# Kernel tuning notes

Measured on AMD Instinct MI355X. Metric: run time of the kernel, lower is better.

The kernel has to match this reference:

```python
import jax, jax.numpy as jnp
import numpy as np

V, D, H, L, S, B, HD, FF, MAXS = 50257, 1024, 8, 6, 1024, 2, 128, 4096, 2048
EPS = 1e-5
STD = 0.02


def rmsnorm(x, w):
    rms = jnp.sqrt(jnp.mean(x * x, axis=-1, keepdims=True) + EPS)
    return w * (x / rms)


def setup_inputs() -> dict:
    key = jax.random.key(0)
    ks = jax.random.split(key, 9)
    return {
        "tokens": jax.random.randint(ks[0], (S, B), 0, V),
        "tok_emb": STD * jax.random.normal(ks[1], (V, D), jnp.float32),
        "pos_emb": STD * jax.random.normal(ks[2], (MAXS, D), jnp.float32),
        "attn_norm_w": jnp.ones((L, D), jnp.float32),
        "Wq": STD * jax.random.normal(ks[3], (L, H, D, HD), jnp.float32),
        "Wk": STD * jax.random.normal(ks[4], (L, H, D, HD), jnp.float32),
        "Wv": STD * jax.random.normal(ks[5], (L, H, D, HD), jnp.float32),
        "Wo": STD * jax.random.normal(ks[6], (L, H, HD, D), jnp.float32),
        "mlp_norm_w": jnp.ones((L, D), jnp.float32),
        "W1": STD * jax.random.normal(ks[7], (L, D, FF), jnp.float32),
        "W2": STD * jax.random.normal(ks[8], (L, FF, D), jnp.float32),
        "final_norm_w": jnp.ones((D,), jnp.float32),
    }


def reference(tokens, tok_emb, pos_emb, attn_norm_w, Wq, Wk, Wv, Wo,
              mlp_norm_w, W1, W2, final_norm_w):
    seq_len = tokens.shape[0]
    scale = HD ** -0.5
    # (S, B, D) token + learned positional embeddings
    x = tok_emb[tokens] + pos_emb[:seq_len][:, None, :]
    causal = jnp.tril(jnp.ones((seq_len, seq_len), bool))  # (S, S)
    for l in range(L):
        n = rmsnorm(x, attn_norm_w[l])
        q = jnp.einsum('sbd,hdk->bhsk', n, Wq[l])
        k = jnp.einsum('sbd,hdk->bhsk', n, Wk[l])
        v = jnp.einsum('sbd,hdk->bhsk', n, Wv[l])
        scores = jnp.einsum('bhsk,bhtk->bhst', q, k) * scale
        scores = jnp.where(causal, scores, -jnp.inf)
        w = jax.nn.softmax(scores, axis=-1)
        attn = jnp.einsum('bhst,bhtk->bhsk', w, v)
        # per-head out_proj summed over heads (matches sum over head modules)
        x = x + jnp.einsum('bhsk,hkd->sbd', attn, Wo[l])
        m = rmsnorm(x, mlp_norm_w[l])
        h = jax.nn.silu(jnp.einsum('sbd,df->sbf', m, W1[l]))
        x = x + jnp.einsum('sbf,fd->sbd', h, W2[l])
    x = rmsnorm(x, final_norm_w)
    logits = jnp.einsum('sbd,vd->sbv', x, tok_emb)  # tied lm_head
    return logits
```

## Files before the change

kernel.cpp:

```cpp
#include <hip/hip_runtime.h>
#include <hip/hip_bf16.h>
#include <cstddef>
#include <cstdint>

#define VOCAB 50257
#define VPAD  50432
#define DMODEL 1024
#define NHEAD 8
#define NLAYER 6
#define SEQ 1024
#define BATCH 2
#define HDIM 128
#define FFDIM 4096
#define NTOK (SEQ * BATCH)
#define QKVLD 3072
#define EPSV 1e-5f


typedef __attribute__((ext_vector_type(8))) short short8;
typedef __attribute__((ext_vector_type(4))) float f32x4;

__device__ __forceinline__ unsigned short f2bf(float f) {
    union { float f; unsigned u; } v; v.f = f;
    unsigned r = v.u + 0x7FFF + ((v.u >> 16) & 1);
    return (unsigned short)(r >> 16);
}

__global__ __launch_bounds__(256) void embed_kernel(
    const int* __restrict__ tokens, const float* __restrict__ tok_emb,
    const float* __restrict__ pos_emb, float* __restrict__ x)
{
    int idx = blockIdx.x * 256 + threadIdx.x;
    int t = idx >> 10;
    int d = idx & (DMODEL - 1);
    int b = t >> 10, s = t & (SEQ - 1);
    int tok = tokens[s * BATCH + b];
    x[idx] = tok_emb[(size_t)tok * DMODEL + d] + pos_emb[(size_t)s * DMODEL + d];
}

__global__ __launch_bounds__(256) void rmsnorm_bf_kernel(
    const float* __restrict__ x, const float* __restrict__ w,
    unsigned short* __restrict__ o)
{
    int t = blockIdx.x;
    int tid = threadIdx.x;
    const float4 xv = ((const float4*)(x + (size_t)t * DMODEL))[tid];
    float ss = xv.x * xv.x + xv.y * xv.y + xv.z * xv.z + xv.w * xv.w;
    __shared__ float red[256];
    red[tid] = ss;
    __syncthreads();
    for (int off = 128; off > 0; off >>= 1) {
        if (tid < off) red[tid] += red[tid + off];
        __syncthreads();
    }
    float inv = rsqrtf(red[0] * (1.0f / DMODEL) + EPSV);
    const float4 wv = ((const float4*)w)[tid];
    ushort4 ov;
    ov.x = f2bf(wv.x * xv.x * inv);
    ov.y = f2bf(wv.y * xv.y * inv);
    ov.z = f2bf(wv.z * xv.z * inv);
    ov.w = f2bf(wv.w * xv.w * inv);
    ((ushort4*)(o + (size_t)t * DMODEL))[tid] = ov;
}

__global__ __launch_bounds__(256) void transpose_cast_kernel(
    const float* __restrict__ in, unsigned short* __restrict__ out, int R, int C)
{
    __shared__ float tile[32][33];
    const size_t bo = (size_t)blockIdx.z * R * C;
    const float* src = in + bo;
    unsigned short* dst = out + bo;
    int c0 = blockIdx.x * 32, r0 = blockIdx.y * 32;
    int tx = threadIdx.x, ty = threadIdx.y;
    #pragma unroll
    for (int i = 0; i < 32; i += 8)
        tile[ty + i][tx] = src[(size_t)(r0 + ty + i) * C + c0 + tx];
    __syncthreads();
    #pragma unroll
    for (int i = 0; i < 32; i += 8)
        dst[(size_t)(c0 + ty + i) * R + r0 + tx] = f2bf(tile[tx][ty + i]);
}

__global__ __launch_bounds__(256) void transpose_qkv_kernel(
    const float* __restrict__ in, unsigned short* __restrict__ out, int row_off)
{
    __shared__ float tile[32][33];
    int z = blockIdx.z;
    int l = z >> 3, h = z & 7;
    const float* src = in + (size_t)z * DMODEL * HDIM;
    unsigned short* dst = out + (size_t)l * QKVLD * DMODEL
                              + (size_t)(row_off + h * HDIM) * DMODEL;
    int c0 = blockIdx.x * 32, r0 = blockIdx.y * 32;
    int tx = threadIdx.x, ty = threadIdx.y;
    #pragma unroll
    for (int i = 0; i < 32; i += 8)
        tile[ty + i][tx] = src[(size_t)(r0 + ty + i) * HDIM + c0 + tx];
    __syncthreads();
    #pragma unroll
    for (int i = 0; i < 32; i += 8)
        dst[(size_t)(c0 + ty + i) * DMODEL + r0 + tx] = f2bf(tile[tx][ty + i]);
}

__global__ __launch_bounds__(256) void vt_transpose_kernel(
    const unsigned short* __restrict__ qkv, unsigned short* __restrict__ vt)
{
    __shared__ unsigned short tile[32][33];
    int c0 = blockIdx.x * 32;
    int r0 = blockIdx.y * 32;
    int tx = threadIdx.x, ty = threadIdx.y;
    #pragma unroll
    for (int i = 0; i < 32; i += 8)
        tile[ty + i][tx] = qkv[(size_t)(r0 + ty + i) * QKVLD + 2048 + c0 + tx];
    __syncthreads();
    #pragma unroll
    for (int i = 0; i < 32; i += 8)
        vt[(size_t)(c0 + ty + i) * NTOK + r0 + tx] = tile[tx][ty + i];
}

__global__ __launch_bounds__(256) void cast_pad_kernel(
    const float* __restrict__ in, unsigned short* __restrict__ out,
    long n_src, long n_tot)
{
    long i = ((long)blockIdx.x * 256 + threadIdx.x) * 8;
    if (i >= n_tot) return;
    short8 o8;
    if (i < n_src) {
        const float4* p = (const float4*)(in + i);
        float4 a = p[0], b = p[1];
        o8[0] = (short)f2bf(a.x); o8[1] = (short)f2bf(a.y);
        o8[2] = (short)f2bf(a.z); o8[3] = (short)f2bf(a.w);
        o8[4] = (short)f2bf(b.x); o8[5] = (short)f2bf(b.y);
        o8[6] = (short)f2bf(b.z); o8[7] = (short)f2bf(b.w);
    } else {
        o8 = (short8)0;
    }
    *(short8*)(out + i) = o8;
}

template<bool ATOMIC, bool SILU, bool BF16OUT>
__global__ __launch_bounds__(256, 2) void mm128_kernel(
    const unsigned short* __restrict__ A, const unsigned short* __restrict__ Bt,
    void* __restrict__ Cv, int M, int N, int K, int rows, int ksplit)
{
    int nwg = gridDim.x;
    int flat = blockIdx.x;
    int q8 = nwg >> 3, r8 = nwg & 7;
    int xcd = flat & 7, lid = flat >> 3;
    int wg = (r8 == 0) ? (xcd * q8 + lid)
           : ((xcd < r8 ? xcd * (q8 + 1) : r8 * (q8 + 1) + (xcd - r8) * q8) + lid);
    int rs = rows * ksplit;
    const int col0 = (wg / rs) * 128;
    int rem = wg % rs;
    const int row0 = (rem / ksplit) * 128;
    const int sk   = rem % ksplit;
    const int Keff = K / ksplit;
    const int kbase = sk * Keff;

    __shared__ __align__(16) char lds[65536];
    const int tid  = threadIdx.x;
    const int lane = tid & 63;
    const int wave = tid >> 6;
    const int wm = wave >> 1, wn = wave & 1;
    const int g  = lane >> 4;
    const int c  = lane & 15;

    f32x4 acc[4][4] = {};

    auto STAGE = [&](int buf, int t) {
        const int k0 = kbase + t * 64;
        char* base = lds + buf * 32768;
        #pragma unroll
        for (int j = 0; j < 4; ++j) {
            int chunk = j * 256 + tid;
            int row = chunk >> 3, slot = chunk & 7;
            int ss = slot ^ (row & 7);
            __builtin_amdgcn_global_load_lds(
                (const __attribute__((address_space(1))) void*)
                    (A + (size_t)(row0 + row) * K + k0 + ss * 8),
                (__attribute__((address_space(3))) void*)(base + chunk * 16), 16, 0, 0);
        }
        #pragma unroll
        for (int j = 0; j < 4; ++j) {
            int chunk = j * 256 + tid;
            int row = chunk >> 3, slot = chunk & 7;
            int ss = slot ^ (row & 7);
            __builtin_amdgcn_global_load_lds(
                (const __attribute__((address_space(1))) void*)
                    (Bt + (size_t)(col0 + row) * K + k0 + ss * 8),
                (__attribute__((address_space(3))) void*)(base + 16384 + chunk * 16), 16, 0, 0);
        }
    };

    const int NT = Keff >> 6;
    STAGE(0, 0);
    asm volatile("s_waitcnt vmcnt(0)" ::: "memory");
    __builtin_amdgcn_s_barrier();
    __builtin_amdgcn_sched_barrier(0);

    for (int t = 0; t < NT; ++t) {
        if (t + 1 < NT) STAGE((t + 1) & 1, t + 1);

        char* base = lds + (t & 1) * 32768;
        short8 af[2][4], bf[2][4];
        #pragma unroll
        for (int ks = 0; ks < 2; ++ks) {
            #pragma unroll
            for (int i = 0; i < 4; ++i) {
                int rowa = wm * 64 + i * 16 + c;
                af[ks][i] = *(const short8*)(base + rowa * 128 + (((ks * 4 + g) ^ (rowa & 7)) << 4));
                int rowb = wn * 64 + i * 16 + c;
                bf[ks][i] = *(const short8*)(base + 16384 + rowb * 128 + (((ks * 4 + g) ^ (rowb & 7)) << 4));
            }
        }
        __builtin_amdgcn_s_setprio(1);
        #pragma unroll
        for (int ks = 0; ks < 2; ++ks)
            #pragma unroll
            for (int i = 0; i < 4; ++i)
                #pragma unroll
                for (int j = 0; j < 4; ++j)
                    acc[i][j] = __builtin_amdgcn_mfma_f32_16x16x32_bf16(
                        af[ks][i], bf[ks][j], acc[i][j], 0, 0, 0);
        __builtin_amdgcn_s_setprio(0);

        if (t + 1 < NT) asm volatile("s_waitcnt vmcnt(0)" ::: "memory");
        __builtin_amdgcn_s_barrier();
        __builtin_amdgcn_sched_barrier(0);
    }

    float* Cf = (float*)Cv;
    unsigned short* Cb = (unsigned short*)Cv;
    const int crow  = row0 + wm * 64 + g * 4;
    const int ccol0 = col0 + wn * 64 + c;
    #pragma unroll
    for (int i = 0; i < 4; ++i) {
        #pragma unroll
        for (int j = 0; j < 4; ++j) {
            int gcol = ccol0 + j * 16;
            #pragma unroll
            for (int r = 0; r < 4; ++r) {
                int grow = crow + i * 16 + r;
                float v = acc[i][j][r];
                if (SILU) v = v / (1.0f + __expf(-v));
                size_t ci = (size_t)grow * N + gcol;
                if (ATOMIC)       atomicAdd(&Cf[ci], v);
                else if (BF16OUT) Cb[ci] = f2bf(v);
                else              Cf[ci] = v;
            }
        }
    }
}

template<bool SILU, bool BF16OUT, int RM>
__global__ __launch_bounds__(512, 1) void mm256_kernel(
    const unsigned short* __restrict__ A, const unsigned short* __restrict__ Bt,
    void* __restrict__ Cv, int M, int N, int K, int rows)
{
    int nwg = gridDim.x;
    int flat = blockIdx.x;
    int q8 = nwg >> 3, r8 = nwg & 7;
    int xcd = flat & 7, lid = flat >> 3;
    int wg = (r8 == 0) ? (xcd * q8 + lid)
           : ((xcd < r8 ? xcd * (q8 + 1) : r8 * (q8 + 1) + (xcd - r8) * q8) + lid);
    const int row0 = (wg % rows) * 256;
    const int col0 = (wg / rows) * 256;

    __shared__ __align__(16) char lds[131072];
    const int tid  = threadIdx.x;
    const int lane = tid & 63;
    const int wave = tid >> 6;
    const int wm = wave >> 2;
    const int wn = wave & 3;
    const int g  = lane >> 4;
    const int c  = lane & 15;

    f32x4 acc[8][4] = {};

    auto STAGE = [&](int buf, int tile) {
        const int k0 = tile * 32;
        char* base = lds + buf * 32768;
        #pragma unroll
        for (int j = 0; j < 2; ++j) {
            int chunk = j * 512 + tid;
            int row = chunk >> 2, slot = chunk & 3;
            int sslot = slot ^ ((row >> 1) & 3);
            __builtin_amdgcn_global_load_lds(
                (const __attribute__((address_space(1))) void*)
                    (A + (size_t)(row0 + row) * K + k0 + sslot * 8),
                (__attribute__((address_space(3))) void*)(base + chunk * 16), 16, 0, 0);
        }
        #pragma unroll
        for (int j = 0; j < 2; ++j) {
            int chunk = j * 512 + tid;
            int row = chunk >> 2, slot = chunk & 3;
            int sslot = slot ^ ((row >> 1) & 3);
            __builtin_amdgcn_global_load_lds(
                (const __attribute__((address_space(1))) void*)
                    (Bt + (size_t)(col0 + row) * K + k0 + sslot * 8),
                (__attribute__((address_space(3))) void*)(base + 16384 + chunk * 16), 16, 0, 0);
        }
    };

    const int NT = K >> 5;
    STAGE(0, 0); STAGE(1, 1); STAGE(2, 2);
    asm volatile("s_waitcnt vmcnt(8)" ::: "memory");
    __builtin_amdgcn_s_barrier();
    __builtin_amdgcn_sched_barrier(0);

    for (int t = 0; t < NT; ++t) {
        if (t + 3 < NT) STAGE((t + 3) & 3, t + 3);

        char* base = lds + (t & 3) * 32768;
        short8 af[8], bf[4];
        #pragma unroll
        for (int mf = 0; mf < 8; ++mf) {
            int row = wm * 128 + mf * 16 + c;
            af[mf] = *(const short8*)(base + row * 64 + ((g ^ ((row >> 1) & 3)) << 4));
        }
        #pragma unroll
        for (int nf = 0; nf < 4; ++nf) {
            int row = wn * 64 + nf * 16 + c;
            bf[nf] = *(const short8*)(base + 16384 + row * 64 + ((g ^ ((row >> 1) & 3)) << 4));
        }
        __builtin_amdgcn_s_setprio(1);
        #pragma unroll
        for (int mf = 0; mf < 8; ++mf)
            #pragma unroll
            for (int nf = 0; nf < 4; ++nf)
                acc[mf][nf] = __builtin_amdgcn_mfma_f32_16x16x32_bf16(
                    af[mf], bf[nf], acc[mf][nf], 0, 0, 0);
        __builtin_amdgcn_s_setprio(0);
        __builtin_amdgcn_sched_barrier(0);

        if (t + 1 < NT) {
            if (t + 3 < NT)      asm volatile("s_waitcnt vmcnt(8)" ::: "memory");
            else if (t + 2 < NT) asm volatile("s_waitcnt vmcnt(4)" ::: "memory");
            else                 asm volatile("s_waitcnt vmcnt(0)" ::: "memory");
            __builtin_amdgcn_s_barrier();
            __builtin_amdgcn_sched_barrier(0);
        }
    }

    float* Cf = (float*)Cv;
    unsigned short* Cb = (unsigned short*)Cv;
    #pragma unroll
    for (int mf = 0; mf < 8; ++mf) {
        #pragma unroll
        for (int nf = 0; nf < 4; ++nf) {
            int gcol = col0 + wn * 64 + nf * 16 + c;
            if (gcol < N) {
                #pragma unroll
                for (int r = 0; r < 4; ++r) {
                    int grow = row0 + wm * 128 + mf * 16 + g * 4 + r;
                    int orow = RM ? (((grow & (SEQ - 1)) << 1) | (grow >> 10)) : grow;
                    float v = acc[mf][nf][r];
                    if (SILU) v = v / (1.0f + __expf(-v));
                    size_t ci = (size_t)orow * N + gcol;
                    if (BF16OUT) Cb[ci] = f2bf(v);
                    else         Cf[ci] = v;
                }
            }
        }
    }
}

__global__ __launch_bounds__(256) void flash_attn_kernel(
    const unsigned short* __restrict__ q, const unsigned short* __restrict__ k,
    const unsigned short* __restrict__ vt, unsigned short* __restrict__ o)
{
    const int qt   = blockIdx.x;
    const int h    = blockIdx.y;
    const int b    = blockIdx.z;
    const int tid  = threadIdx.x;
    const int lane = tid & 63;
    const int wave = tid >> 6;
    const int g    = lane >> 4;
    const int c    = lane & 15;

    __shared__ unsigned short k_lds[64 * 128];
    __shared__ unsigned short vt_lds[128 * 64];
    __shared__ unsigned short p_lds[4 * 16 * 64];

    const int q0  = qt * 64;
    const int wq0 = q0 + wave * 16;
    const int tokb = b * SEQ;

    short8 qf[4];
    {
        const unsigned short* qr =
            q + (size_t)(tokb + wq0 + c) * QKVLD + h * HDIM + g * 8;
        #pragma unroll
        for (int dblk = 0; dblk < 4; ++dblk)
            qf[dblk] = *(const short8*)(qr + dblk * 32);
    }

    f32x4 oacc[8] = {};
    float m = -1e30f, l = 0.f;
    const float scale = 0.08838834764831845f;
    const int myq = wq0 + c;

    const int nt = qt + 1;
    for (int it = 0; it < nt; ++it) {
        const int kv0 = it * 64;
        short8 kc[4], vc[4];
        #pragma unroll
        for (int i = 0; i < 4; ++i) {
            int chunk = tid + i * 256;
            int key = chunk >> 4, cc = chunk & 15;
            kc[i] = *(const short8*)(
                k + (size_t)(tokb + kv0 + key) * QKVLD + h * HDIM + cc * 8);
        }
        #pragma unroll
        for (int i = 0; i < 4; ++i) {
            int chunk = tid + i * 256;
            int d = chunk >> 3, cc = chunk & 7;
            vc[i] = *(const short8*)(
                vt + (size_t)(h * HDIM + d) * NTOK + tokb + kv0 + cc * 8);
        }
        __syncthreads();
        #pragma unroll
        for (int i = 0; i < 4; ++i) {
            int chunk = tid + i * 256;
            int key = chunk >> 4, cc = chunk & 15;
            *(short8*)((char*)k_lds + ((key * 256 + cc * 16) ^ ((key & 7) << 4))) = kc[i];
        }
        #pragma unroll
        for (int i = 0; i < 4; ++i) {
            int chunk = tid + i * 256;
            int d = chunk >> 3, cc = chunk & 7;
            *(short8*)((char*)vt_lds + ((d * 128 + cc * 16) ^ ((d & 7) << 4))) = vc[i];
        }
        __syncthreads();

        f32x4 st[4];
        #pragma unroll
        for (int sub = 0; sub < 4; ++sub) {
            f32x4 acc = {};
            int key = sub * 16 + c;
            #pragma unroll
            for (int dblk = 0; dblk < 4; ++dblk) {
                short8 kf = *(const short8*)((char*)k_lds +
                    ((key * 256 + dblk * 64 + g * 16) ^ ((key & 7) << 4)));
                acc = __builtin_amdgcn_mfma_f32_16x16x32_bf16(kf, qf[dblk], acc, 0, 0, 0);
            }
            st[sub] = acc;
        }

        #pragma unroll
        for (int sub = 0; sub < 4; ++sub)
            #pragma unroll
            for (int r = 0; r < 4; ++r) {
                int key = kv0 + sub * 16 + g * 4 + r;
                float s = st[sub][r] * scale;
                st[sub][r] = (key <= myq) ? s : -1e30f;
            }

        float tm = -1e30f;
        #pragma unroll
        for (int sub = 0; sub < 4; ++sub)
            #pragma unroll
            for (int r = 0; r < 4; ++r) tm = fmaxf(tm, st[sub][r]);
        tm = fmaxf(tm, __shfl_xor(tm, 16));
        tm = fmaxf(tm, __shfl_xor(tm, 32));
        float mnew = fmaxf(m, tm);
        float sc_f = __expf(m - mnew);
        m = mnew;

        float ps = 0.f;
        #pragma unroll
        for (int sub = 0; sub < 4; ++sub) {
            float p0 = __expf(st[sub][0] - m);
            float p1 = __expf(st[sub][1] - m);
            float p2 = __expf(st[sub][2] - m);
            float p3 = __expf(st[sub][3] - m);
            ps += (p0 + p1) + (p2 + p3);
            ushort4 pk;
            pk.x = f2bf(p0); pk.y = f2bf(p1); pk.z = f2bf(p2); pk.w = f2bf(p3);
            *(ushort4*)((char*)p_lds + wave * 2048 +
                ((c * 128 + sub * 32 + g * 8) ^ ((c & 7) << 4))) = pk;
        }
        ps += __shfl_xor(ps, 16);
        ps += __shfl_xor(ps, 32);
        l = l * sc_f + ps;
        #pragma unroll
        for (int dt = 0; dt < 8; ++dt)
            #pragma unroll
            for (int r = 0; r < 4; ++r) oacc[dt][r] *= sc_f;

        #pragma unroll
        for (int kb = 0; kb < 2; ++kb) {
            short8 pf = *(const short8*)((char*)p_lds + wave * 2048 +
                ((c * 128 + kb * 64 + g * 16) ^ ((c & 7) << 4)));
            #pragma unroll
            for (int dt = 0; dt < 8; ++dt) {
                int d = dt * 16 + c;
                short8 vf = *(const short8*)((char*)vt_lds +
                    ((d * 128 + kb * 64 + g * 16) ^ ((d & 7) << 4)));
                oacc[dt] = __builtin_amdgcn_mfma_f32_16x16x32_bf16(vf, pf, oacc[dt], 0, 0, 0);
            }
        }
    }

    float inv = 1.0f / l;
    unsigned short* orow = o + (size_t)(tokb + wq0 + c) * DMODEL + h * HDIM + g * 4;
    #pragma unroll
    for (int dt = 0; dt < 8; ++dt) {
        ushort4 ov;
        ov.x = f2bf(oacc[dt][0] * inv);
        ov.y = f2bf(oacc[dt][1] * inv);
        ov.z = f2bf(oacc[dt][2] * inv);
        ov.w = f2bf(oacc[dt][3] * inv);
        *(ushort4*)(orow + dt * 16) = ov;
    }
}

extern "C" void kernel_launch(void* const* d_in, const int* in_sizes, int n_in,
                              void* d_out, int out_size, void* d_ws, size_t ws_size,
                              hipStream_t stream)
{
    const int*   tokens       = (const int*)  d_in[0];
    const float* tok_emb      = (const float*)d_in[1];
    const float* pos_emb      = (const float*)d_in[2];
    const float* attn_norm_w  = (const float*)d_in[3];
    const float* Wq           = (const float*)d_in[4];
    const float* Wk           = (const float*)d_in[5];
    const float* Wv           = (const float*)d_in[6];
    const float* Wo           = (const float*)d_in[7];
    const float* mlp_norm_w   = (const float*)d_in[8];
    const float* W1           = (const float*)d_in[9];
    const float* W2           = (const float*)d_in[10];
    const float* final_norm_w = (const float*)d_in[11];
    float* out = (float*)d_out;

    char* wp = (char*)d_ws;
    size_t off = 0;
    auto alloc = [&](size_t bytes) -> void* {
        void* p = wp + off;
        off += (bytes + 255) & ~(size_t)255;
        return p;
    };
    float* x             = (float*)alloc((size_t)NTOK * DMODEL * 4);
    unsigned short* nbf     = (unsigned short*)alloc((size_t)NTOK * DMODEL * 2);
    unsigned short* qkvbf   = (unsigned short*)alloc((size_t)NTOK * QKVLD * 2);
    unsigned short* vtb     = (unsigned short*)alloc((size_t)DMODEL * NTOK * 2);
    unsigned short* attnbf  = (unsigned short*)alloc((size_t)NTOK * DMODEL * 2);
    unsigned short* hbf     = (unsigned short*)alloc((size_t)NTOK * FFDIM * 2);
    unsigned short* temb    = (unsigned short*)alloc((size_t)VPAD * DMODEL * 2);
    unsigned short* Wqkv_t  = (unsigned short*)alloc((size_t)NLAYER * QKVLD * DMODEL * 2);
    unsigned short* Wo_t    = (unsigned short*)alloc((size_t)NLAYER * DMODEL * DMODEL * 2);
    unsigned short* W1_t    = (unsigned short*)alloc((size_t)NLAYER * DMODEL * FFDIM * 2);
    unsigned short* W2_t    = (unsigned short*)alloc((size_t)NLAYER * FFDIM * DMODEL * 2);
    if (off > ws_size) return;

    {
        dim3 bb(32, 8), g(HDIM / 32, DMODEL / 32, NLAYER * NHEAD);
        transpose_qkv_kernel<<<g, bb, 0, stream>>>(Wq, Wqkv_t, 0);
        transpose_qkv_kernel<<<g, bb, 0, stream>>>(Wk, Wqkv_t, DMODEL);
        transpose_qkv_kernel<<<g, bb, 0, stream>>>(Wv, Wqkv_t, 2 * DMODEL);
    }
    {
        dim3 bb(32, 8), g(DMODEL / 32, DMODEL / 32, NLAYER);
        transpose_cast_kernel<<<g, bb, 0, stream>>>(Wo, Wo_t, DMODEL, DMODEL);
    }
    {
        dim3 bb(32, 8), g(FFDIM / 32, DMODEL / 32, NLAYER);
        transpose_cast_kernel<<<g, bb, 0, stream>>>(W1, W1_t, DMODEL, FFDIM);
    }
    {
        dim3 bb(32, 8), g(DMODEL / 32, FFDIM / 32, NLAYER);
        transpose_cast_kernel<<<g, bb, 0, stream>>>(W2, W2_t, FFDIM, DMODEL);
    }
    {
        long n_src = (long)VOCAB * DMODEL, n_tot = (long)VPAD * DMODEL;
        cast_pad_kernel<<<(unsigned)(n_tot / 8 / 256), 256, 0, stream>>>(
            tok_emb, temb, n_src, n_tot);
    }

    embed_kernel<<<(NTOK * DMODEL) / 256, 256, 0, stream>>>(tokens, tok_emb, pos_emb, x);

    const size_t LW    = (size_t)DMODEL * DMODEL;
    const size_t LWQKV = (size_t)QKVLD * DMODEL;
    const size_t LWF   = (size_t)DMODEL * FFDIM;

    for (int l = 0; l < NLAYER; l++) {
        rmsnorm_bf_kernel<<<NTOK, 256, 0, stream>>>(x, attn_norm_w + (size_t)l * DMODEL, nbf);
        mm128_kernel<false, false, true><<<384, 256, 0, stream>>>(
            nbf, Wqkv_t + l * LWQKV, qkvbf, NTOK, QKVLD, DMODEL, 16, 1);
        vt_transpose_kernel<<<dim3(DMODEL / 32, NTOK / 32), dim3(32, 8), 0, stream>>>(
            qkvbf, vtb);
        flash_attn_kernel<<<dim3(SEQ / 64, NHEAD, BATCH), 256, 0, stream>>>(
            qkvbf, qkvbf + DMODEL, vtb, attnbf);
        mm128_kernel<true, false, false><<<8 * 16 * 2, 256, 0, stream>>>(
            attnbf, Wo_t + l * LW, x, NTOK, DMODEL, DMODEL, 16, 2);
        rmsnorm_bf_kernel<<<NTOK, 256, 0, stream>>>(x, mlp_norm_w + (size_t)l * DMODEL, nbf);
        mm128_kernel<false, true, true><<<32 * 16, 256, 0, stream>>>(
            nbf, W1_t + l * LWF, hbf, NTOK, FFDIM, DMODEL, 16, 1);
        mm128_kernel<true, false, false><<<8 * 16 * 2, 256, 0, stream>>>(
            hbf, W2_t + l * LWF, x, NTOK, DMODEL, FFDIM, 16, 2);
    }

    rmsnorm_bf_kernel<<<NTOK, 256, 0, stream>>>(x, final_norm_w, nbf);
    mm256_kernel<false, false, 1><<<8 * 197, 512, 0, stream>>>(
        nbf, temb, out, NTOK, VOCAB, DMODEL, 8);
}
```

Before: 1.415 ms.

## Deepen mm128 GEMM pipeline to four LDS stages with K-tile of 32

New measurement: 1.415 ms. No clear change (-0.0%).

```diff
diff --git a/kernel.cpp b/kernel.cpp
--- a/kernel.cpp
+++ b/kernel.cpp
@@ -137,7 +137,7 @@
     *(short8*)(out + i) = o8;
 }
 
-template<bool ATOMIC, bool SILU, bool BF16OUT>
+template<bool ATOMIC, bool SILU, bool BF16OUT, int RM>
 __global__ __launch_bounds__(256, 2) void mm128_kernel(
     const unsigned short* __restrict__ A, const unsigned short* __restrict__ Bt,
     void* __restrict__ Cv, int M, int N, int K, int rows, int ksplit)
@@ -167,65 +167,69 @@
     f32x4 acc[4][4] = {};
 
     auto STAGE = [&](int buf, int t) {
-        const int k0 = kbase + t * 64;
-        char* base = lds + buf * 32768;
-        #pragma unroll
-        for (int j = 0; j < 4; ++j) {
+        const int k0 = kbase + t * 32;
+        char* base = lds + buf * 16384;
+        #pragma unroll
+        for (int j = 0; j < 2; ++j) {
             int chunk = j * 256 + tid;
-            int row = chunk >> 3, slot = chunk & 7;
-            int ss = slot ^ (row & 7);
+            int row = chunk >> 2, slot = chunk & 3;
+            int ss = slot ^ ((row >> 1) & 3);
             __builtin_amdgcn_global_load_lds(
                 (const __attribute__((address_space(1))) void*)
                     (A + (size_t)(row0 + row) * K + k0 + ss * 8),
                 (__attribute__((address_space(3))) void*)(base + chunk * 16), 16, 0, 0);
         }
         #pragma unroll
-        for (int j = 0; j < 4; ++j) {
+        for (int j = 0; j < 2; ++j) {
             int chunk = j * 256 + tid;
-            int row = chunk >> 3, slot = chunk & 7;
-            int ss = slot ^ (row & 7);
+            int row = chunk >> 2, slot = chunk & 3;
+            int ss = slot ^ ((row >> 1) & 3);
             __builtin_amdgcn_global_load_lds(
                 (const __attribute__((address_space(1))) void*)
                     (Bt + (size_t)(col0 + row) * K + k0 + ss * 8),
-                (__attribute__((address_space(3))) void*)(base + 16384 + chunk * 16), 16, 0, 0);
+                (__attribute__((address_space(3))) void*)(base + 8192 + chunk * 16), 16, 0, 0);
         }
     };
 
-    const int NT = Keff >> 6;
+    const int NT = Keff >> 5;
     STAGE(0, 0);
-    asm volatile("s_waitcnt vmcnt(0)" ::: "memory");
+    if (NT > 1) STAGE(1, 1);
+    if (NT > 2) STAGE(2, 2);
+    if (NT > 2)      asm volatile("s_waitcnt vmcnt(8)" ::: "memory");
+    else if (NT > 1) asm volatile("s_waitcnt vmcnt(4)" ::: "memory");
+    else             asm volatile("s_waitcnt vmcnt(0)" ::: "memory");
     __builtin_amdgcn_s_barrier();
     __builtin_amdgcn_sched_barrier(0);
 
     for (int t = 0; t < NT; ++t) {
-        if (t + 1 < NT) STAGE((t + 1) & 1, t + 1);
-
-        char* base = lds + (t & 1) * 32768;
-        short8 af[2][4], bf[2][4];
-        #pragma unroll
-        for (int ks = 0; ks < 2; ++ks) {
+        if (t + 3 < NT) STAGE((t + 3) & 3, t + 3);
+
+        char* base = lds + (t & 3) * 16384;
+        short8 af[4], bf[4];
+        #pragma unroll
+        for (int i = 0; i < 4; ++i) {
+            int rowa = wm * 64 + i * 16 + c;
+            af[i] = *(const short8*)(base + rowa * 64 + ((g ^ ((rowa >> 1) & 3)) << 4));
+            int rowb = wn * 64 + i * 16 + c;
+            bf[i] = *(const short8*)(base + 8192 + rowb * 64 + ((g ^ ((rowb >> 1) & 3)) << 4));
+        }
+        __builtin_amdgcn_s_setprio(1);
+        #pragma unroll
+        for (int i = 0; i < 4; ++i)
             #pragma unroll
-            for (int i = 0; i < 4; ++i) {
-                int rowa = wm * 64 + i * 16 + c;
-                af[ks][i] = *(const short8*)(base + rowa * 128 + (((ks * 4 + g) ^ (rowa & 7)) << 4));
-                int rowb = wn * 64 + i * 16 + c;
-                bf[ks][i] = *(const short8*)(base + 16384 + rowb * 128 + (((ks * 4 + g) ^ (rowb & 7)) << 4));
-            }
-        }
-        __builtin_amdgcn_s_setprio(1);
-        #pragma unroll
-        for (int ks = 0; ks < 2; ++ks)
-            #pragma unroll
-            for (int i = 0; i < 4; ++i)
-                #pragma unroll
-                for (int j = 0; j < 4; ++j)
-                    acc[i][j] = __builtin_amdgcn_mfma_f32_16x16x32_bf16(
-                        af[ks][i], bf[ks][j], acc[i][j], 0, 0, 0);
+            for (int j = 0; j < 4; ++j)
+                acc[i][j] = __builtin_amdgcn_mfma_f32_16x16x32_bf16(
+                    af[i], bf[j], acc[i][j], 0, 0, 0);
         __builtin_amdgcn_s_setprio(0);
-
-        if (t + 1 < NT) asm volatile("s_waitcnt vmcnt(0)" ::: "memory");
-        __builtin_amdgcn_s_barrier();
         __builtin_amdgcn_sched_barrier(0);
+
+        if (t + 1 < NT) {
+            if (t + 3 < NT)      asm volatile("s_waitcnt vmcnt(8)" ::: "memory");
+            else if (t + 2 < NT) asm volatile("s_waitcnt vmcnt(4)" ::: "memory");
+            else                 asm volatile("s_waitcnt vmcnt(0)" ::: "memory");
+            __builtin_amdgcn_s_barrier();
+            __builtin_amdgcn_sched_barrier(0);
+        }
     }
 
     float* Cf = (float*)Cv;
@@ -237,15 +241,18 @@
         #pragma unroll
         for (int j = 0; j < 4; ++j) {
             int gcol = ccol0 + j * 16;
-            #pragma unroll
-            for (int r = 0; r < 4; ++r) {
-                int grow = crow + i * 16 + r;
-                float v = acc[i][j][r];
-                if (SILU) v = v / (1.0f + __expf(-v));
-                size_t ci = (size_t)grow * N + gcol;
-                if (ATOMIC)       atomicAdd(&Cf[ci], v);
-                else if (BF16OUT) Cb[ci] = f2bf(v);
-                else              Cf[ci] = v;
+            if (gcol < N) {
+                #pragma unroll
+                for (int r = 0; r < 4; ++r) {
+                    int grow = crow + i * 16 + r;
+                    int orow = RM ? (((grow & (SEQ - 1)) << 1) | (grow >> 10)) : grow;
+                    float v = acc[i][j][r];
+                    if (SILU) v = v / (1.0f + __expf(-v));
+                    size_t ci = (size_t)orow * N + gcol;
+                    if (ATOMIC)       atomicAdd(&Cf[ci], v);
+                    else if (BF16OUT) Cb[ci] = f2bf(v);
+                    else              Cf[ci] = v;
+                }
             }
         }
     }
@@ -584,18 +591,18 @@
 
     for (int l = 0; l < NLAYER; l++) {
         rmsnorm_bf_kernel<<<NTOK, 256, 0, stream>>>(x, attn_norm_w + (size_t)l * DMODEL, nbf);
-        mm128_kernel<false, false, true><<<384, 256, 0, stream>>>(
+        mm128_kernel<false, false, true, 0><<<384, 256, 0, stream>>>(
             nbf, Wqkv_t + l * LWQKV, qkvbf, NTOK, QKVLD, DMODEL, 16, 1);
         vt_transpose_kernel<<<dim3(DMODEL / 32, NTOK / 32), dim3(32, 8), 0, stream>>>(
             qkvbf, vtb);
         flash_attn_kernel<<<dim3(SEQ / 64, NHEAD, BATCH), 256, 0, stream>>>(
             qkvbf, qkvbf + DMODEL, vtb, attnbf);
-        mm128_kernel<true, false, false><<<8 * 16 * 2, 256, 0, stream>>>(
+        mm128_kernel<true, false, false, 0><<<8 * 16 * 2, 256, 0, stream>>>(
             attnbf, Wo_t + l * LW, x, NTOK, DMODEL, DMODEL, 16, 2);
         rmsnorm_bf_kernel<<<NTOK, 256, 0, stream>>>(x, mlp_norm_w + (size_t)l * DMODEL, nbf);
-        mm128_kernel<false, true, true><<<32 * 16, 256, 0, stream>>>(
+        mm128_kernel<false, true, true, 0><<<32 * 16, 256, 0, stream>>>(
             nbf, W1_t + l * LWF, hbf, NTOK, FFDIM, DMODEL, 16, 1);
-        mm128_kernel<true, false, false><<<8 * 16 * 2, 256, 0, stream>>>(
+        mm128_kernel<true, false, false, 0><<<8 * 16 * 2, 256, 0, stream>>>(
             hbf, W2_t + l * LWF, x, NTOK, DMODEL, FFDIM, 16, 2);
     }
 
```
